# Kernel tuning notes

Measured on AMD Instinct MI355X. Metric: run time of the kernel, lower is better.

The kernel has to match this reference:

```python
import jax, jax.numpy as jnp
import numpy as np

V = 32          # num_variables
T = 48          # num_time_bins
D = 512         # d_model
H = 8           # num_heads
HD = D // H     # head_dim = 64
OD = 16         # observation_dim
B = 4


def setup_inputs() -> dict:
    key = jax.random.key(0)
    ks = jax.random.split(key, 20)
    s = 0.02
    inp = {
        'h': jax.random.normal(ks[0], (B, T, V, D), jnp.float32),
        'observation_state': jax.random.normal(ks[1], (B, T, V, 2), jnp.float32),
        'Wq': jax.random.normal(ks[2], (D, D), jnp.float32) * s,
        'bq': jnp.zeros((D,), jnp.float32),
        'Wk': jax.random.normal(ks[3], (D, D), jnp.float32) * s,
        'bk': jnp.zeros((D,), jnp.float32),
        'Wv': jax.random.normal(ks[4], (D, D), jnp.float32) * s,
        'bv': jnp.zeros((D,), jnp.float32),
        'Wo': jax.random.normal(ks[5], (D, D), jnp.float32) * s,
        'bo': jnp.zeros((D,), jnp.float32),
        'Woq': jax.random.normal(ks[6], (2, H * OD), jnp.float32) * 0.5,
        'boq': jnp.zeros((H * OD,), jnp.float32),
        'Wok': jax.random.normal(ks[7], (2, H * OD), jnp.float32) * 0.5,
        'bok': jnp.zeros((H * OD,), jnp.float32),
        'variable_bias': jax.random.normal(ks[8], (H, V, V), jnp.float32) * 0.01,
        'relative_time_bias': jax.random.normal(ks[9], (H, 2 * T - 1), jnp.float32) * 0.01,
    }
    return inp


def reference(h, observation_state, Wq, bq, Wk, bk, Wv, bv, Wo, bo,
              Woq, boq, Wok, bok, variable_bias, relative_time_bias):
    N = T * V
    scale = 1.0 / np.sqrt(HD)
    obs_scale = 1.0 / np.sqrt(OD)

    # static index buffers (constants)
    flat_var_ids = jnp.tile(jnp.arange(V), T)                       # [N]
    flat_time_ids = jnp.repeat(jnp.arange(T), V)                    # [N]
    rel_index = flat_time_ids[:, None] - flat_time_ids[None, :] + (T - 1)  # [N,N]

    fh = h.reshape(B, N, D)
    fo = observation_state.reshape(B, N, 2)

    def heads(x, nh, hd):
        return x.reshape(B, N, nh, hd).transpose(0, 2, 1, 3)  # [B,H,N,hd]

    q = heads(fh @ Wq + bq, H, HD)
    k = heads(fh @ Wk + bk, H, HD)
    v = heads(fh @ Wv + bv, H, HD)
    oq = heads(fo @ Woq + boq, H, OD)
    ok = heads(fo @ Wok + bok, H, OD)

    content = jnp.einsum('bhnd,bhmd->bhnm', q, k) * scale
    obs = jnp.einsum('bhnd,bhmd->bhnm', oq, ok) * obs_scale
    var_scores = variable_bias[:, flat_var_ids[:, None], flat_var_ids[None, :]]  # [H,N,N]
    time_scores = relative_time_bias[:, rel_index]                                # [H,N,N]

    scores = content + obs + var_scores[None] + time_scores[None]
    attn = jax.nn.softmax(scores, axis=-1)  # dropout off (inference)
    out = jnp.einsum('bhnm,bhmd->bhnd', attn, v)
    out = out.transpose(0, 2, 1, 3).reshape(B, N, D)
    out = out @ Wo + bo
    return out.reshape(B, T, V, D)
```

## Files before the change

### kernel.cpp

```cpp
#include <hip/hip_runtime.h>
#include <math.h>

typedef __bf16 bf16x8 __attribute__((ext_vector_type(8)));
typedef float f32x4 __attribute__((ext_vector_type(4)));

#define NB 4
#define NT 48
#define NV 32
#define ND 512
#define NH 8
#define NN 1536
#define NBN 6144
#define L2E 1.44269504f

#define GLOAD_LDS(g, l) \
    __builtin_amdgcn_global_load_lds( \
        (const __attribute__((address_space(1))) void*)(g), \
        (__attribute__((address_space(3))) void*)(l), 16, 0, 0)

__global__ __launch_bounds__(256) void prep(
    const float* __restrict__ h, const float* __restrict__ obs,
    const float* __restrict__ Wq, const float* __restrict__ Wk,
    const float* __restrict__ Wv, const float* __restrict__ Wo,
    const float* __restrict__ bq, const float* __restrict__ bk,
    const float* __restrict__ bv,
    const float* __restrict__ Wok, const float* __restrict__ bok,
    __bf16* __restrict__ h_bf, __bf16* __restrict__ WcatT,
    __bf16* __restrict__ WoT, float* __restrict__ biascat,
    __bf16* __restrict__ kx)
{
    __shared__ float ts[64][68];
    const int tid = threadIdx.x;
    const int bx = blockIdx.x;
    if (bx < 1536) {
        int t = bx * 256 + tid;
        const float4* src = (const float4*)h + (size_t)t * 2;
        float4 a = src[0], b = src[1];
        __bf16 r[8] = {(__bf16)a.x, (__bf16)a.y, (__bf16)a.z, (__bf16)a.w,
                       (__bf16)b.x, (__bf16)b.y, (__bf16)b.z, (__bf16)b.w};
        *(uint4*)(h_bf + (size_t)t * 8) = *(uint4*)r;
    } else if (bx < 1792) {
        int bw = bx - 1536;
        const int p = bw >> 6, tile = bw & 63;
        const int k0 = (tile >> 3) * 64, c0 = (tile & 7) * 64;
        const float* W = (p == 0) ? Wq : (p == 1) ? Wk : (p == 2) ? Wv : Wo;
        const float scale = (p == 0) ? 0.125f * L2E : 1.0f;
        #pragma unroll
        for (int i = 0; i < 4; i++) {
            int r = (tid >> 4) + i * 16;
            float4 v = *(const float4*)(W + (size_t)(k0 + r) * 512 + c0 + (tid & 15) * 4);
            *(float4*)&ts[r][(tid & 15) * 4] = v;
        }
        __syncthreads();
        __bf16 tmp[16];
        #pragma unroll
        for (int j = 0; j < 16; j++)
            tmp[j] = (__bf16)(ts[(tid & 3) * 16 + j][tid >> 2] * scale);
        int crow = c0 + (tid >> 2);
        __bf16* dst = (p < 3)
            ? WcatT + ((size_t)(p * 512 + crow)) * 512 + k0 + (tid & 3) * 16
            : WoT   + ((size_t)crow) * 512 + k0 + (tid & 3) * 16;
        *(uint4*)dst = *(uint4*)tmp;
        *(uint4*)(dst + 8) = *(uint4*)(tmp + 8);
        if (p < 3 && k0 == 0 && tid < 64) {
            const float* bb = (p == 0) ? bq : (p == 1) ? bk : bv;
            biascat[p * 512 + c0 + tid] = bb[c0 + tid] * scale;
        }
    } else {
        int t = (bx - 1792) * 256 + tid;
        int row = t >> 1, half = t & 1;
        __bf16* dst = kx + (size_t)row * 96 + 64 + half * 16;
        if (half == 0) {
            int bh = row / NN, n = row - bh * NN;
            int b = bh >> 3, hh = bh & 7;
            size_t bn = (size_t)b * NN + n;
            float o0 = obs[bn * 2], o1 = obs[bn * 2 + 1];
            int f = hh * 16;
            __bf16 tmp[16];
            #pragma unroll
            for (int j = 0; j < 16; j++)
                tmp[j] = (__bf16)(o0 * Wok[f + j] + o1 * Wok[128 + f + j] + bok[f + j]);
            *(uint4*)dst       = *(uint4*)tmp;
            *(uint4*)(dst + 8) = *(uint4*)(tmp + 8);
        } else {
            uint4 z = {0, 0, 0, 0};
            *(uint4*)dst       = z;
            *(uint4*)(dst + 8) = z;
        }
    }
}

template<int TM, bool BF16OUT>
__global__ __launch_bounds__(256) void gemm_mfma(
    const __bf16* __restrict__ A, const __bf16* __restrict__ Bt,
    const float* __restrict__ bias, float* __restrict__ Cf,
    __bf16* __restrict__ qarr, __bf16* __restrict__ kx,
    __bf16* __restrict__ vt)
{
    constexpr int MT = TM / 32;
    __shared__ __align__(16) char smem[34816];
    char* const As0 = smem;
    char* const As1 = smem + TM * 64;
    char* const Bs0 = smem + TM * 128;
    char* const Bs1 = smem + TM * 128 + 8192;
    const int tid = threadIdx.x;
    const int w = tid >> 6, lane = tid & 63;
    const int quad = lane >> 4, l16 = lane & 15;
    const int wm = w >> 1, wn = w & 1;
    const int n0 = blockIdx.x * 128, m0 = blockIdx.y * TM;

    const int sm = tid >> 2;
    const int sk = ((tid & 3) ^ ((sm >> 1) & 3)) * 8;
    const __bf16* aptr = A  + (size_t)(m0 + sm) * 512 + sk;
    const __bf16* bptr = Bt + (size_t)(n0 + sm) * 512 + sk;

    f32x4 zero4 = {0.f, 0.f, 0.f, 0.f};
    f32x4 acc[MT][4];
    #pragma unroll
    for (int i = 0; i < MT; i++)
        #pragma unroll
        for (int j = 0; j < 4; j++) acc[i][j] = zero4;

    auto STAGE = [&](char* dA, char* dB, int kt) {
        GLOAD_LDS(aptr + kt, dA + tid * 16);
        if (TM == 128) GLOAD_LDS(aptr + 64 * 512 + kt, dA + 4096 + tid * 16);
        GLOAD_LDS(bptr + kt, dB + tid * 16);
        GLOAD_LDS(bptr + 64 * 512 + kt, dB + 4096 + tid * 16);
    };
    auto COMPUTE = [&](const char* Asb, const char* Bsb) {
        bf16x8 af[MT], bfr[4];
        #pragma unroll
        for (int mt = 0; mt < MT; mt++) {
            int rr = wm * (TM / 2) + mt * 16 + l16;
            af[mt] = *(const bf16x8*)(Asb + rr * 64 + (quad ^ ((rr >> 1) & 3)) * 16);
        }
        #pragma unroll
        for (int nt = 0; nt < 4; nt++) {
            int rr = wn * 64 + nt * 16 + l16;
            bfr[nt] = *(const bf16x8*)(Bsb + rr * 64 + (quad ^ ((rr >> 1) & 3)) * 16);
        }
        #pragma unroll
        for (int mt = 0; mt < MT; mt++)
            #pragma unroll
            for (int nt = 0; nt < 4; nt++)
                acc[mt][nt] = __builtin_amdgcn_mfma_f32_16x16x32_bf16(
                    af[mt], bfr[nt], acc[mt][nt], 0, 0, 0);
    };

    STAGE(As0, Bs0, 0);
    asm volatile("s_waitcnt vmcnt(0)" ::: "memory");
    __builtin_amdgcn_s_barrier();
    for (int kt = 0; kt < 512; kt += 64) {
        STAGE(As1, Bs1, kt + 32);
        COMPUTE(As0, Bs0);
        asm volatile("s_waitcnt vmcnt(0)" ::: "memory");
        __builtin_amdgcn_s_barrier();
        if (kt + 64 < 512) STAGE(As0, Bs0, kt + 64);
        COMPUTE(As1, Bs1);
        asm volatile("s_waitcnt vmcnt(0)" ::: "memory");
        __builtin_amdgcn_s_barrier();
    }

    __syncthreads();
    if (BF16OUT) {
        if (n0 >= 1024) {
            __bf16* CsT = (__bf16*)smem;
            #pragma unroll
            for (int nt = 0; nt < 4; nt++) {
                int cl = wn * 64 + nt * 16 + l16;
                float bia = bias[n0 + cl];
                #pragma unroll
                for (int mt = 0; mt < MT; mt++) {
                    int rl0 = wm * (TM / 2) + mt * 16 + quad * 4;
                    __bf16 pk[4];
                    #pragma unroll
                    for (int r = 0; r < 4; r++)
                        pk[r] = (__bf16)(acc[mt][nt][r] + bia);
                    *(uint2*)&CsT[cl * 136 + rl0] = *(uint2*)pk;
                }
            }
            __syncthreads();
            int cl = tid >> 1, half = tid & 1;
            int f0 = (n0 + cl) & 511;
            int hh = f0 >> 6, d = f0 & 63;
            int dt = d >> 4, l16v = d & 15;
            int bidx = m0 / NN, nm = m0 - bidx * NN;
            int bh = bidx * 8 + hh;
            int mtv = (nm >> 6) + half;
            __bf16* dstb = vt + ((size_t)(bh * 24 + mtv)) * 4096 + l16v * 8;
            #pragma unroll
            for (int j = 0; j < 8; j++) {
                uint4 v = *(uint4*)&CsT[cl * 136 + half * 64 + j * 8];
                int frag = dt * 2 + (j >> 2), qd = j & 3;
                *(uint4*)(dstb + (frag * 4 + qd) * 128) = v;
            }
        } else {
            __bf16* Cs = (__bf16*)smem;
            #pragma unroll
            for (int mt = 0; mt < MT; mt++)
                #pragma unroll
                for (int nt = 0; nt < 4; nt++) {
                    int cl = wn * 64 + nt * 16 + l16;
                    float bia = bias[n0 + cl];
                    #pragma unroll
                    for (int r = 0; r < 4; r++) {
                        int rl = wm * (TM / 2) + mt * 16 + quad * 4 + r;
                        Cs[rl * 132 + cl] = (__bf16)(acc[mt][nt][r] + bia);
                    }
                }
            __syncthreads();
            int rl = tid >> 1, hb = tid & 1;
            int grow = m0 + rl;
            int col0 = n0 + hb * 64;
            int p = col0 >> 9, f0 = col0 & 511, hh = f0 >> 6;
            int bidx = grow / NN, n = grow - bidx * NN;
            __bf16* dst = (p == 0) ? qarr + (size_t)grow * 512 + f0
                                   : kx + ((size_t)(bidx * 8 + hh) * NN + n) * 96;
            #pragma unroll
            for (int j = 0; j < 8; j++) {
                uint2 lo = *(uint2*)&Cs[rl * 132 + hb * 64 + j * 8];
                uint2 hi = *(uint2*)&Cs[rl * 132 + hb * 64 + j * 8 + 4];
                uint4 v = {lo.x, lo.y, hi.x, hi.y};
                *(uint4*)(dst + j * 8) = v;
            }
        }
    } else {
        float* Csf = (float*)smem;
        #pragma unroll
        for (int mt = 0; mt < MT; mt++)
            #pragma unroll
            for (int nt = 0; nt < 4; nt++) {
                int cl = wn * 64 + nt * 16 + l16;
                float bia = bias[n0 + cl];
                #pragma unroll
                for (int r = 0; r < 4; r++) {
                    int rl = wm * (TM / 2) + mt * 16 + quad * 4 + r;
                    Csf[rl * 132 + cl] = acc[mt][nt][r] + bia;
                }
            }
        __syncthreads();
        int rl = tid >> 2, q4 = tid & 3;
        float* dst = Cf + (size_t)(m0 + rl) * 512 + n0 + q4 * 32;
        #pragma unroll
        for (int j = 0; j < 8; j++) {
            uint4 v = *(uint4*)&Csf[rl * 132 + q4 * 32 + j * 4];
            *(uint4*)(dst + j * 4) = v;
        }
    }
}

__global__ __launch_bounds__(256) void attn_mfma(
    const __bf16* __restrict__ qarr, const __bf16* __restrict__ kx,
    const __bf16* __restrict__ vt, const float* __restrict__ obs,
    const float* __restrict__ Woq, const float* __restrict__ boq,
    const float* __restrict__ varb, const float* __restrict__ rtb,
    __bf16* __restrict__ aout)
{
    __shared__ __align__(16) __bf16 Ks[64][128];
    __shared__ __align__(16) __bf16 Ps[64][64];
    __shared__ float rts[96];

    const int tid = threadIdx.x;
    const int w = tid >> 6, lane = tid & 63;
    const int quad = lane >> 4, l16 = lane & 15;
    const int bh = blockIdx.x, qt = blockIdx.y;
    const int b = bh >> 3, h = bh & 7;
    const int n0 = qt * 64;

    if (tid < 95) rts[tid] = rtb[h * 95 + tid] * L2E;

    const int ck = (tid & 15) ^ ((tid >> 4) & 7);
    const __bf16* kbase = kx + (size_t)bh * NN * 96 + ck * 8;
    const __bf16* vtile = vt + (size_t)bh * 24 * 4096 + lane * 8;

    auto STAGE_K = [&](int m0s) {
        #pragma unroll
        for (int i = 0; i < 4; i++) {
            int row = i * 16 + (tid >> 4);
            GLOAD_LDS(kbase + (size_t)(m0s + row) * 96,
                      (char*)Ks + i * 4096 + tid * 16);
        }
    };

    STAGE_K(0);

    const int nl = w * 16 + l16;
    const size_t qrow = (size_t)(b * NN + n0 + nl);
    bf16x8 bq_[3];
    bq_[0] = *(const bf16x8*)(qarr + qrow * 512 + h * 64 + quad * 8);
    bq_[1] = *(const bf16x8*)(qarr + qrow * 512 + h * 64 + 32 + quad * 8);
    {
        uint4 a2u = {0u, 0u, 0u, 0u};
        if (quad < 2) {
            float o0 = obs[qrow * 2], o1 = obs[qrow * 2 + 1];
            int f = h * 16 + quad * 8;
            const float sc = 0.25f * L2E;
            __bf16 tmp[8];
            #pragma unroll
            for (int j = 0; j < 8; j++)
                tmp[j] = (__bf16)(sc * (o0 * Woq[f + j] + o1 * Woq[128 + f + j]
                                        + boq[f + j]));
            a2u = *(uint4*)tmp;
        }
        bq_[2] = *(bf16x8*)&a2u;
    }

    const int rm = (w & 1) * 16 + l16;
    float4 vbA = *(const float4*)(varb + h * 1024 + rm * 32 + quad * 4);
    float4 vbB = *(const float4*)(varb + h * 1024 + rm * 32 + 16 + quad * 4);
    float vA[4] = {vbA.x * L2E, vbA.y * L2E, vbA.z * L2E, vbA.w * L2E};
    float vB[4] = {vbB.x * L2E, vbB.y * L2E, vbB.z * L2E, vbB.w * L2E};
    const int tn = 2 * qt + (w >> 1);

    int wo2[4], ro2[2];
    #pragma unroll
    for (int ct = 0; ct < 4; ct++)
        wo2[ct] = (((ct * 2 + (quad >> 1)) ^ (nl & 7)) * 16) + (quad & 1) * 8;
    #pragma unroll
    for (int ks = 0; ks < 2; ks++)
        ro2[ks] = ((ks * 4 + quad) ^ (nl & 7)) * 16;
    char* psrow = (char*)Ps + nl * 128;

    f32x4 zero4 = {0.f, 0.f, 0.f, 0.f};
    f32x4 o[4];
    f32x4 lpv = zero4;
    #pragma unroll
    for (int i = 0; i < 4; i++) o[i] = zero4;

    asm volatile("s_waitcnt vmcnt(0) lgkmcnt(0)" ::: "memory");
    __builtin_amdgcn_s_barrier();

    for (int mt = 0; mt < 24; mt++) {
        const __bf16* vtm = vtile + (size_t)mt * 4096;
        bf16x8 vfr[4][2];
        #pragma unroll
        for (int dt = 0; dt < 4; dt++)
            #pragma unroll
            for (int ks = 0; ks < 2; ks++)
                vfr[dt][ks] = *(const bf16x8*)(vtm + (dt * 2 + ks) * 512);

        f32x4 sc[4];
        __builtin_amdgcn_s_setprio(1);
        #pragma unroll
        for (int ct = 0; ct < 4; ct++) {
            f32x4 d = zero4;
            int row = ct * 16 + l16;
            #pragma unroll
            for (int ks = 0; ks < 3; ks++) {
                bf16x8 kf = *(const bf16x8*)((const char*)Ks + row * 256
                                + (((ks * 4 + quad) ^ (row & 7)) * 16));
                d = __builtin_amdgcn_mfma_f32_16x16x32_bf16(kf, bq_[ks], d, 0, 0, 0);
            }
            sc[ct] = d;
        }
        __builtin_amdgcn_s_setprio(0);

        asm volatile("s_waitcnt lgkmcnt(0)" ::: "memory");
        __builtin_amdgcn_s_barrier();

        if (mt + 1 < 24) STAGE_K((mt + 1) * 64);

        float tb0 = rts[tn - 2 * mt + 47];
        float tb1 = rts[tn - 2 * mt + 46];
        #pragma unroll
        for (int ct = 0; ct < 4; ct++) {
            float tb = (ct & 2) ? tb1 : tb0;
            const float* vv = (ct & 1) ? vB : vA;
            __bf16 pk[4];
            #pragma unroll
            for (int r = 0; r < 4; r++) {
                float p = exp2f(sc[ct][r] + tb + vv[r]);
                lpv[r] += p;
                pk[r] = (__bf16)p;
            }
            *(uint2*)(psrow + wo2[ct]) = *(uint2*)pk;
        }

        __builtin_amdgcn_s_setprio(1);
        #pragma unroll
        for (int ks = 0; ks < 2; ks++) {
            bf16x8 pf = *(const bf16x8*)(psrow + ro2[ks]);
            #pragma unroll
            for (int dt = 0; dt < 4; dt++)
                o[dt] = __builtin_amdgcn_mfma_f32_16x16x32_bf16(
                    vfr[dt][ks], pf, o[dt], 0, 0, 0);
        }
        __builtin_amdgcn_s_setprio(0);

        asm volatile("s_waitcnt vmcnt(0)" ::: "memory");
        __builtin_amdgcn_s_barrier();
    }

    float lp = (lpv[0] + lpv[1]) + (lpv[2] + lpv[3]);
    lp += __shfl_xor(lp, 16);
    lp += __shfl_xor(lp, 32);
    float inv = 1.0f / lp;
    size_t abase = ((size_t)b * NN + n0 + nl) * 512 + h * 64 + quad * 4;
    #pragma unroll
    for (int dt = 0; dt < 4; dt++) {
        __bf16 ov[4];
        #pragma unroll
        for (int r = 0; r < 4; r++) ov[r] = (__bf16)(o[dt][r] * inv);
        *(uint2*)(aout + abase + dt * 16) = *(uint2*)ov;
    }
}

extern "C" void kernel_launch(void* const* d_in, const int* in_sizes, int n_in,
                              void* d_out, int out_size, void* d_ws, size_t ws_size,
                              hipStream_t stream)
{
    const float* h_   = (const float*)d_in[0];
    const float* obs  = (const float*)d_in[1];
    const float* Wq   = (const float*)d_in[2];
    const float* bq   = (const float*)d_in[3];
    const float* Wk   = (const float*)d_in[4];
    const float* bk   = (const float*)d_in[5];
    const float* Wv   = (const float*)d_in[6];
    const float* bv   = (const float*)d_in[7];
    const float* Wo   = (const float*)d_in[8];
    const float* bo   = (const float*)d_in[9];
    const float* Woq  = (const float*)d_in[10];
    const float* boq  = (const float*)d_in[11];
    const float* Wok  = (const float*)d_in[12];
    const float* bok  = (const float*)d_in[13];
    const float* varb = (const float*)d_in[14];
    const float* rtb  = (const float*)d_in[15];
    float* out = (float*)d_out;

    char* ws = (char*)d_ws;
    __bf16* h_bf    = (__bf16*)ws;                 ws += (size_t)NBN * 512 * 2;
    __bf16* qarr    = (__bf16*)ws;                 ws += (size_t)NBN * 512 * 2;
    __bf16* vt      = (__bf16*)ws;                 ws += (size_t)NBN * 512 * 2;
    __bf16* kx      = (__bf16*)ws;                 ws += ((size_t)32 * NN * 96 + 64) * 2;
    __bf16* attnout = (__bf16*)ws;                 ws += (size_t)NBN * 512 * 2;
    __bf16* WcatT   = (__bf16*)ws;                 ws += (size_t)1536 * 512 * 2;
    __bf16* WoT    = (__bf16*)ws;                  ws += (size_t)512 * 512 * 2;
    float*  biascat = (float*)ws;                  ws += 1536 * 4;

    prep<<<dim3(2176), dim3(256), 0, stream>>>(
        h_, obs, Wq, Wk, Wv, Wo, bq, bk, bv, Wok, bok,
        h_bf, WcatT, WoT, biascat, kx);
    gemm_mfma<128, true><<<dim3(12, 48), dim3(256), 0, stream>>>(
        h_bf, WcatT, biascat, nullptr, qarr, kx, vt);
    attn_mfma<<<dim3(32, 24), dim3(256), 0, stream>>>(qarr, kx, vt, obs, Woq, boq,
                                                      varb, rtb, attnout);
    gemm_mfma<64, false><<<dim3(4, 96), dim3(256), 0, stream>>>(
        attnout, WoT, bo, out, nullptr, nullptr, nullptr);
}
```

Baseline: 181.7 us.

## Split attention keys across waves with register-resident K/V fragments and LDS reduction

Rewrites the attention kernel so each wave handles a different 16-key slice of every key tile across all 64 queries, instead of 16 queries across all keys. K and V are written by the producer kernels in a pre-fragmented layout that each lane loads straight into registers with software prefetch, which removes LDS staging of K and P and the per-iteration barriers. Partial outputs and row sums are reduced across the four waves through LDS at the end. The cost is more registers per thread (four query fragments, sixteen output accumulators) and a serialized final reduction, which may lower occupancy.

```diff
diff --git a/kernel.cpp b/kernel.cpp
--- a/kernel.cpp
+++ b/kernel.cpp
@@ -3,6 +3,7 @@
 
 typedef __bf16 bf16x8 __attribute__((ext_vector_type(8)));
 typedef float f32x4 __attribute__((ext_vector_type(4)));
+typedef short short4v __attribute__((ext_vector_type(4)));
 
 #define NB 4
 #define NT 48
@@ -69,10 +70,13 @@
     } else {
         int t = (bx - 1792) * 256 + tid;
         int row = t >> 1, half = t & 1;
-        __bf16* dst = kx + (size_t)row * 96 + 64 + half * 16;
+        int bh = row / NN, n = row - bh * NN;
+        int mt = n >> 6, wv = (n >> 4) & 3, l16k = n & 15;
+        __bf16* dst = kx + (((size_t)(bh * 24 + mt) * 4 + wv) * 3 + 2) * 512
+                         + (half * 2) * 128 + l16k * 8;
         if (half == 0) {
-            int bh = row / NN, n = row - bh * NN;
-            int b = bh >> 3, hh = bh & 7;
+            int hh = bh & 7;
+            int b = bh >> 3;
             size_t bn = (size_t)b * NN + n;
             float o0 = obs[bn * 2], o1 = obs[bn * 2 + 1];
             int f = hh * 16;
@@ -80,12 +84,12 @@
             #pragma unroll
             for (int j = 0; j < 16; j++)
                 tmp[j] = (__bf16)(o0 * Wok[f + j] + o1 * Wok[128 + f + j] + bok[f + j]);
-            *(uint4*)dst       = *(uint4*)tmp;
-            *(uint4*)(dst + 8) = *(uint4*)(tmp + 8);
+            *(uint4*)dst         = *(uint4*)tmp;
+            *(uint4*)(dst + 128) = *(uint4*)(tmp + 8);
         } else {
             uint4 z = {0, 0, 0, 0};
-            *(uint4*)dst       = z;
-            *(uint4*)(dst + 8) = z;
+            *(uint4*)dst         = z;
+            *(uint4*)(dst + 128) = z;
         }
     }
 }
@@ -187,12 +191,14 @@
             int bidx = m0 / NN, nm = m0 - bidx * NN;
             int bh = bidx * 8 + hh;
             int mtv = (nm >> 6) + half;
-            __bf16* dstb = vt + ((size_t)(bh * 24 + mtv)) * 4096 + l16v * 8;
             #pragma unroll
             for (int j = 0; j < 8; j++) {
                 uint4 v = *(uint4*)&CsT[cl * 136 + half * 64 + j * 8];
-                int frag = dt * 2 + (j >> 2), qd = j & 3;
-                *(uint4*)(dstb + (frag * 4 + qd) * 128) = v;
+                __bf16* pp = (__bf16*)&v;
+                size_t fo = (((size_t)(bh * 24 + mtv) * 4 + (j >> 1)) * 4 + dt) * 256;
+                int q0 = (j & 1) * 2;
+                *(uint2*)(vt + fo + q0 * 64 + l16v * 4)       = *(uint2*)&pp[0];
+                *(uint2*)(vt + fo + (q0 + 1) * 64 + l16v * 4) = *(uint2*)&pp[4];
             }
         } else {
             __bf16* Cs = (__bf16*)smem;
@@ -214,14 +220,25 @@
             int col0 = n0 + hb * 64;
             int p = col0 >> 9, f0 = col0 & 511, hh = f0 >> 6;
             int bidx = grow / NN, n = grow - bidx * NN;
-            __bf16* dst = (p == 0) ? qarr + (size_t)grow * 512 + f0
-                                   : kx + ((size_t)(bidx * 8 + hh) * NN + n) * 96;
-            #pragma unroll
-            for (int j = 0; j < 8; j++) {
-                uint2 lo = *(uint2*)&Cs[rl * 132 + hb * 64 + j * 8];
-                uint2 hi = *(uint2*)&Cs[rl * 132 + hb * 64 + j * 8 + 4];
-                uint4 v = {lo.x, lo.y, hi.x, hi.y};
-                *(uint4*)(dst + j * 8) = v;
+            if (p == 0) {
+                __bf16* dst = qarr + (size_t)grow * 512 + f0;
+                #pragma unroll
+                for (int j = 0; j < 8; j++) {
+                    uint2 lo = *(uint2*)&Cs[rl * 132 + hb * 64 + j * 8];
+                    uint2 hi = *(uint2*)&Cs[rl * 132 + hb * 64 + j * 8 + 4];
+                    uint4 v = {lo.x, lo.y, hi.x, hi.y};
+                    *(uint4*)(dst + j * 8) = v;
+                }
+            } else {
+                int mtk = n >> 6, wv = (n >> 4) & 3, l16k = n & 15;
+                size_t fb = ((size_t)((bidx * 8 + hh) * 24 + mtk) * 4 + wv) * 1536;
+                #pragma unroll
+                for (int j = 0; j < 8; j++) {
+                    uint2 lo = *(uint2*)&Cs[rl * 132 + hb * 64 + j * 8];
+                    uint2 hi = *(uint2*)&Cs[rl * 132 + hb * 64 + j * 8 + 4];
+                    uint4 v = {lo.x, lo.y, hi.x, hi.y};
+                    *(uint4*)(kx + fb + (j >> 2) * 512 + (j & 3) * 128 + l16k * 8) = v;
+                }
             }
         }
     } else {
@@ -256,9 +273,9 @@
     const float* __restrict__ varb, const float* __restrict__ rtb,
     __bf16* __restrict__ aout)
 {
-    __shared__ __align__(16) __bf16 Ks[64][128];
-    __shared__ __align__(16) __bf16 Ps[64][64];
-    __shared__ float rts[96];
+    __shared__ float Or[64][68];
+    __shared__ float lps[4][64];
+    __shared__ float2 rts2[96];
 
     const int tid = threadIdx.x;
     const int w = tid >> 6, lane = tid & 63;
@@ -267,142 +284,158 @@
     const int b = bh >> 3, h = bh & 7;
     const int n0 = qt * 64;
 
-    if (tid < 95) rts[tid] = rtb[h * 95 + tid] * L2E;
-
-    const int ck = (tid & 15) ^ ((tid >> 4) & 7);
-    const __bf16* kbase = kx + (size_t)bh * NN * 96 + ck * 8;
-    const __bf16* vtile = vt + (size_t)bh * 24 * 4096 + lane * 8;
-
-    auto STAGE_K = [&](int m0s) {
-        #pragma unroll
-        for (int i = 0; i < 4; i++) {
-            int row = i * 16 + (tid >> 4);
-            GLOAD_LDS(kbase + (size_t)(m0s + row) * 96,
-                      (char*)Ks + i * 4096 + tid * 16);
-        }
-    };
-
-    STAGE_K(0);
-
-    const int nl = w * 16 + l16;
-    const size_t qrow = (size_t)(b * NN + n0 + nl);
-    bf16x8 bq_[3];
-    bq_[0] = *(const bf16x8*)(qarr + qrow * 512 + h * 64 + quad * 8);
-    bq_[1] = *(const bf16x8*)(qarr + qrow * 512 + h * 64 + 32 + quad * 8);
-    {
+    if (tid < 95) {
+        float a = rtb[h * 95 + tid] * L2E;
+        float c = (tid < 94) ? rtb[h * 95 + tid + 1] * L2E : 0.f;
+        rts2[tid].x = a;
+        rts2[tid].y = c;
+    }
+
+    const __bf16* kwb = kx + ((size_t)bh * 24 * 4 + w) * 1536 + lane * 8;
+    const __bf16* vwb = vt + ((size_t)bh * 24 * 4 + w) * 1024 + lane * 4;
+
+    bf16x8 qf[4][3];
+    #pragma unroll
+    for (int nt = 0; nt < 4; nt++) {
+        const size_t qrow = (size_t)(b * NN + n0 + nt * 16 + l16);
+        qf[nt][0] = *(const bf16x8*)(qarr + qrow * 512 + h * 64 + quad * 8);
+        qf[nt][1] = *(const bf16x8*)(qarr + qrow * 512 + h * 64 + 32 + quad * 8);
         uint4 a2u = {0u, 0u, 0u, 0u};
         if (quad < 2) {
             float o0 = obs[qrow * 2], o1 = obs[qrow * 2 + 1];
             int f = h * 16 + quad * 8;
-            const float sc = 0.25f * L2E;
+            const float scq = 0.25f * L2E;
             __bf16 tmp[8];
             #pragma unroll
             for (int j = 0; j < 8; j++)
-                tmp[j] = (__bf16)(sc * (o0 * Woq[f + j] + o1 * Woq[128 + f + j]
-                                        + boq[f + j]));
+                tmp[j] = (__bf16)(scq * (o0 * Woq[f + j] + o1 * Woq[128 + f + j]
+                                         + boq[f + j]));
             a2u = *(uint4*)tmp;
         }
-        bq_[2] = *(bf16x8*)&a2u;
-    }
-
-    const int rm = (w & 1) * 16 + l16;
-    float4 vbA = *(const float4*)(varb + h * 1024 + rm * 32 + quad * 4);
-    float4 vbB = *(const float4*)(varb + h * 1024 + rm * 32 + 16 + quad * 4);
-    float vA[4] = {vbA.x * L2E, vbA.y * L2E, vbA.z * L2E, vbA.w * L2E};
-    float vB[4] = {vbB.x * L2E, vbB.y * L2E, vbB.z * L2E, vbB.w * L2E};
-    const int tn = 2 * qt + (w >> 1);
-
-    int wo2[4], ro2[2];
-    #pragma unroll
-    for (int ct = 0; ct < 4; ct++)
-        wo2[ct] = (((ct * 2 + (quad >> 1)) ^ (nl & 7)) * 16) + (quad & 1) * 8;
-    #pragma unroll
-    for (int ks = 0; ks < 2; ks++)
-        ro2[ks] = ((ks * 4 + quad) ^ (nl & 7)) * 16;
-    char* psrow = (char*)Ps + nl * 128;
+        qf[nt][2] = *(bf16x8*)&a2u;
+    }
+
+    const float* vbp = varb + h * 1024 + (w & 1) * 16 + quad * 4;
+    f32x4 vvA = *(const f32x4*)(vbp + l16 * 32);
+    f32x4 vvB = *(const f32x4*)(vbp + (16 + l16) * 32);
+    vvA *= L2E; vvB *= L2E;
+
+    const int rbase = 2 * qt - (w >> 1) + 47;
 
     f32x4 zero4 = {0.f, 0.f, 0.f, 0.f};
-    f32x4 o[4];
-    f32x4 lpv = zero4;
-    #pragma unroll
-    for (int i = 0; i < 4; i++) o[i] = zero4;
-
-    asm volatile("s_waitcnt vmcnt(0) lgkmcnt(0)" ::: "memory");
-    __builtin_amdgcn_s_barrier();
+    f32x4 o_p[4][4];
+    #pragma unroll
+    for (int i = 0; i < 4; i++)
+        #pragma unroll
+        for (int j = 0; j < 4; j++) o_p[i][j] = zero4;
+    float lp_s[4] = {0.f, 0.f, 0.f, 0.f};
+
+    bf16x8 kc[3]; short4v vc[4];
+    #pragma unroll
+    for (int ks = 0; ks < 3; ks++) kc[ks] = *(const bf16x8*)(kwb + ks * 512);
+    #pragma unroll
+    for (int dt = 0; dt < 4; dt++) vc[dt] = *(const short4v*)(vwb + dt * 256);
+
+    __syncthreads();
 
     for (int mt = 0; mt < 24; mt++) {
-        const __bf16* vtm = vtile + (size_t)mt * 4096;
-        bf16x8 vfr[4][2];
-        #pragma unroll
-        for (int dt = 0; dt < 4; dt++)
-            #pragma unroll
-            for (int ks = 0; ks < 2; ks++)
-                vfr[dt][ks] = *(const bf16x8*)(vtm + (dt * 2 + ks) * 512);
+        bf16x8 kn[3]; short4v vn[4];
+        if (mt + 1 < 24) {
+            const __bf16* kp = kwb + (size_t)(mt + 1) * 6144;
+            const __bf16* vp = vwb + (size_t)(mt + 1) * 4096;
+            #pragma unroll
+            for (int ks = 0; ks < 3; ks++) kn[ks] = *(const bf16x8*)(kp + ks * 512);
+            #pragma unroll
+            for (int dt = 0; dt < 4; dt++) vn[dt] = *(const short4v*)(vp + dt * 256);
+        }
 
         f32x4 sc[4];
         __builtin_amdgcn_s_setprio(1);
         #pragma unroll
-        for (int ct = 0; ct < 4; ct++) {
+        for (int nt = 0; nt < 4; nt++) {
             f32x4 d = zero4;
-            int row = ct * 16 + l16;
-            #pragma unroll
-            for (int ks = 0; ks < 3; ks++) {
-                bf16x8 kf = *(const bf16x8*)((const char*)Ks + row * 256
-                                + (((ks * 4 + quad) ^ (row & 7)) * 16));
-                d = __builtin_amdgcn_mfma_f32_16x16x32_bf16(kf, bq_[ks], d, 0, 0, 0);
+            #pragma unroll
+            for (int ks = 0; ks < 3; ks++)
+                d = __builtin_amdgcn_mfma_f32_16x16x32_bf16(kc[ks], qf[nt][ks], d, 0, 0, 0);
+            sc[nt] = d;
+        }
+        __builtin_amdgcn_s_setprio(0);
+
+        float2 tb = rts2[rbase - 2 * mt];
+        short4v pf[4];
+        #pragma unroll
+        for (int nt = 0; nt < 4; nt++) {
+            float tbx = (nt < 2) ? tb.x : tb.y;
+            const f32x4& vv = (nt & 1) ? vvB : vvA;
+            union { __bf16 e[4]; short4v s; } pk;
+            #pragma unroll
+            for (int r = 0; r < 4; r++) {
+                float p = exp2f(sc[nt][r] + vv[r] + tbx);
+                lp_s[nt] += p;
+                pk.e[r] = (__bf16)p;
             }
-            sc[ct] = d;
-        }
+            pf[nt] = pk.s;
+        }
+
+        __builtin_amdgcn_s_setprio(1);
+        #pragma unroll
+        for (int nt = 0; nt < 4; nt++)
+            #pragma unroll
+            for (int dt = 0; dt < 4; dt++)
+                o_p[dt][nt] = __builtin_amdgcn_mfma_f32_16x16x16bf16_1k(
+                    vc[dt], pf[nt], o_p[dt][nt], 0, 0, 0);
         __builtin_amdgcn_s_setprio(0);
 
-        asm volatile("s_waitcnt lgkmcnt(0)" ::: "memory");
-        __builtin_amdgcn_s_barrier();
-
-        if (mt + 1 < 24) STAGE_K((mt + 1) * 64);
-
-        float tb0 = rts[tn - 2 * mt + 47];
-        float tb1 = rts[tn - 2 * mt + 46];
-        #pragma unroll
-        for (int ct = 0; ct < 4; ct++) {
-            float tb = (ct & 2) ? tb1 : tb0;
-            const float* vv = (ct & 1) ? vB : vA;
-            __bf16 pk[4];
-            #pragma unroll
-            for (int r = 0; r < 4; r++) {
-                float p = exp2f(sc[ct][r] + tb + vv[r]);
-                lpv[r] += p;
-                pk[r] = (__bf16)p;
-            }
-            *(uint2*)(psrow + wo2[ct]) = *(uint2*)pk;
-        }
-
-        __builtin_amdgcn_s_setprio(1);
-        #pragma unroll
-        for (int ks = 0; ks < 2; ks++) {
-            bf16x8 pf = *(const bf16x8*)(psrow + ro2[ks]);
+        if (mt + 1 < 24) {
+            #pragma unroll
+            for (int ks = 0; ks < 3; ks++) kc[ks] = kn[ks];
+            #pragma unroll
+            for (int dt = 0; dt < 4; dt++) vc[dt] = vn[dt];
+        }
+    }
+
+    #pragma unroll
+    for (int nt = 0; nt < 4; nt++) {
+        lp_s[nt] += __shfl_xor(lp_s[nt], 16);
+        lp_s[nt] += __shfl_xor(lp_s[nt], 32);
+    }
+    if (quad == 0) {
+        #pragma unroll
+        for (int nt = 0; nt < 4; nt++) lps[w][nt * 16 + l16] = lp_s[nt];
+    }
+
+    #pragma unroll
+    for (int ws = 0; ws < 4; ws++) {
+        if (w == ws) {
             #pragma unroll
             for (int dt = 0; dt < 4; dt++)
-                o[dt] = __builtin_amdgcn_mfma_f32_16x16x32_bf16(
-                    vfr[dt][ks], pf, o[dt], 0, 0, 0);
-        }
-        __builtin_amdgcn_s_setprio(0);
-
-        asm volatile("s_waitcnt vmcnt(0)" ::: "memory");
-        __builtin_amdgcn_s_barrier();
-    }
-
-    float lp = (lpv[0] + lpv[1]) + (lpv[2] + lpv[3]);
-    lp += __shfl_xor(lp, 16);
-    lp += __shfl_xor(lp, 32);
-    float inv = 1.0f / lp;
-    size_t abase = ((size_t)b * NN + n0 + nl) * 512 + h * 64 + quad * 4;
-    #pragma unroll
-    for (int dt = 0; dt < 4; dt++) {
-        __bf16 ov[4];
-        #pragma unroll
-        for (int r = 0; r < 4; r++) ov[r] = (__bf16)(o[dt][r] * inv);
-        *(uint2*)(aout + abase + dt * 16) = *(uint2*)ov;
-    }
+                #pragma unroll
+                for (int nt = 0; nt < 4; nt++) {
+                    float* dst = &Or[nt * 16 + l16][dt * 16 + quad * 4];
+                    if (ws == 0) *(f32x4*)dst = o_p[dt][nt];
+                    else {
+                        f32x4 t = *(f32x4*)dst;
+                        *(f32x4*)dst = t + o_p[dt][nt];
+                    }
+                }
+        }
+        __syncthreads();
+    }
+
+    int n = tid >> 2, dq = tid & 3;
+    float linv = 1.0f / (lps[0][n] + lps[1][n] + lps[2][n] + lps[3][n]);
+    __bf16 ov[16];
+    #pragma unroll
+    for (int jj = 0; jj < 4; jj++) {
+        f32x4 t = *(f32x4*)&Or[n][dq * 16 + jj * 4];
+        ov[jj * 4 + 0] = (__bf16)(t[0] * linv);
+        ov[jj * 4 + 1] = (__bf16)(t[1] * linv);
+        ov[jj * 4 + 2] = (__bf16)(t[2] * linv);
+        ov[jj * 4 + 3] = (__bf16)(t[3] * linv);
+    }
+    size_t abase = ((size_t)(b * NN) + n0 + n) * 512 + h * 64 + dq * 16;
+    *(uint4*)(aout + abase)     = *(uint4*)&ov[0];
+    *(uint4*)(aout + abase + 8) = *(uint4*)&ov[8];
 }
 
 extern "C" void kernel_launch(void* const* d_in, const int* in_sizes, int n_in,
@@ -434,7 +467,7 @@
     __bf16* kx      = (__bf16*)ws;                 ws += ((size_t)32 * NN * 96 + 64) * 2;
     __bf16* attnout = (__bf16*)ws;                 ws += (size_t)NBN * 512 * 2;
     __bf16* WcatT   = (__bf16*)ws;                 ws += (size_t)1536 * 512 * 2;
-    __bf16* WoT    = (__bf16*)ws;                  ws += (size_t)512 * 512 * 2;
+    __bf16* WoT     = (__bf16*)ws;                 ws += (size_t)512 * 512 * 2;
     float*  biascat = (float*)ws;                  ws += 1536 * 4;
 
     prep<<<dim3(2176), dim3(256), 0, stream>>>(
```

Result: slower. 186.3 us (+2.5%).

## Keep P in registers via 16x16x16 MFMA, double-buffer K tiles, MFMA row-sum

Applied to the files above, without the earlier changes.

The attention kernel stops writing softmax probabilities to LDS and reading them back. It instead feeds the QK accumulator registers directly as the B operand of 16x16x16 bf16 MFMAs, and the V-transpose layout written by the QKV GEMM is changed to match. K tiles are now double-buffered in LDS, processing two 64-key tiles per barrier pair. The softmax denominator is computed with an MFMA against a ones vector instead of shuffles. The trade-offs are twice as many smaller MFMA instructions, more LDS for K, and a launch-bounds occupancy hint.

```diff
diff --git a/kernel.cpp b/kernel.cpp
--- a/kernel.cpp
+++ b/kernel.cpp
@@ -3,6 +3,8 @@
 
 typedef __bf16 bf16x8 __attribute__((ext_vector_type(8)));
 typedef float f32x4 __attribute__((ext_vector_type(4)));
+typedef short short4v __attribute__((ext_vector_type(4)));
+typedef short short8v __attribute__((ext_vector_type(8)));
 
 #define NB 4
 #define NT 48
@@ -187,12 +189,15 @@
             int bidx = m0 / NN, nm = m0 - bidx * NN;
             int bh = bidx * 8 + hh;
             int mtv = (nm >> 6) + half;
-            __bf16* dstb = vt + ((size_t)(bh * 24 + mtv)) * 4096 + l16v * 8;
             #pragma unroll
             for (int j = 0; j < 8; j++) {
                 uint4 v = *(uint4*)&CsT[cl * 136 + half * 64 + j * 8];
-                int frag = dt * 2 + (j >> 2), qd = j & 3;
-                *(uint4*)(dstb + (frag * 4 + qd) * 128) = v;
+                __bf16* pp = (__bf16*)&v;
+                int q0 = (j & 1) * 2;
+                size_t fo = ((size_t)(bh * 24 + mtv) * 8 + (j >> 1) * 2 + (dt >> 1)) * 512
+                            + (dt & 1) * 4 + l16v * 8;
+                *(uint2*)(vt + fo + q0 * 128)       = *(uint2*)&pp[0];
+                *(uint2*)(vt + fo + (q0 + 1) * 128) = *(uint2*)&pp[4];
             }
         } else {
             __bf16* Cs = (__bf16*)smem;
@@ -249,15 +254,14 @@
     }
 }
 
-__global__ __launch_bounds__(256) void attn_mfma(
+__global__ __launch_bounds__(256, 3) void attn_mfma(
     const __bf16* __restrict__ qarr, const __bf16* __restrict__ kx,
     const __bf16* __restrict__ vt, const float* __restrict__ obs,
     const float* __restrict__ Woq, const float* __restrict__ boq,
     const float* __restrict__ varb, const float* __restrict__ rtb,
     __bf16* __restrict__ aout)
 {
-    __shared__ __align__(16) __bf16 Ks[64][128];
-    __shared__ __align__(16) __bf16 Ps[64][64];
+    __shared__ __align__(16) __bf16 Ks[2][64][128];
     __shared__ float rts[96];
 
     const int tid = threadIdx.x;
@@ -271,18 +275,18 @@
 
     const int ck = (tid & 15) ^ ((tid >> 4) & 7);
     const __bf16* kbase = kx + (size_t)bh * NN * 96 + ck * 8;
-    const __bf16* vtile = vt + (size_t)bh * 24 * 4096 + lane * 8;
-
-    auto STAGE_K = [&](int m0s) {
+    auto STAGE_K = [&](int p, int m0s) {
         #pragma unroll
         for (int i = 0; i < 4; i++) {
             int row = i * 16 + (tid >> 4);
             GLOAD_LDS(kbase + (size_t)(m0s + row) * 96,
-                      (char*)Ks + i * 4096 + tid * 16);
-        }
-    };
-
-    STAGE_K(0);
+                      (char*)Ks + p * 16384 + i * 4096 + tid * 16);
+        }
+    };
+    STAGE_K(0, 0);
+    STAGE_K(1, 64);
+
+    const __bf16* vwb = vt + (size_t)bh * 24 * 4096 + lane * 8;
 
     const int nl = w * 16 + l16;
     const size_t qrow = (size_t)(b * NN + n0 + nl);
@@ -312,34 +316,18 @@
     float vB[4] = {vbB.x * L2E, vbB.y * L2E, vbB.z * L2E, vbB.w * L2E};
     const int tn = 2 * qt + (w >> 1);
 
-    int wo2[4], ro2[2];
+    union { __bf16 e[4]; short4v s; } one_u;
     #pragma unroll
-    for (int ct = 0; ct < 4; ct++)
-        wo2[ct] = (((ct * 2 + (quad >> 1)) ^ (nl & 7)) * 16) + (quad & 1) * 8;
+    for (int j = 0; j < 4; j++) one_u.e[j] = (__bf16)1.0f;
+    const short4v ones = one_u.s;
+
+    f32x4 zero4 = {0.f, 0.f, 0.f, 0.f};
+    f32x4 o_p[4];
+    f32x4 lpa = zero4;
     #pragma unroll
-    for (int ks = 0; ks < 2; ks++)
-        ro2[ks] = ((ks * 4 + quad) ^ (nl & 7)) * 16;
-    char* psrow = (char*)Ps + nl * 128;
-
-    f32x4 zero4 = {0.f, 0.f, 0.f, 0.f};
-    f32x4 o[4];
-    f32x4 lpv = zero4;
-    #pragma unroll
-    for (int i = 0; i < 4; i++) o[i] = zero4;
-
-    asm volatile("s_waitcnt vmcnt(0) lgkmcnt(0)" ::: "memory");
-    __builtin_amdgcn_s_barrier();
-
-    for (int mt = 0; mt < 24; mt++) {
-        const __bf16* vtm = vtile + (size_t)mt * 4096;
-        bf16x8 vfr[4][2];
-        #pragma unroll
-        for (int dt = 0; dt < 4; dt++)
-            #pragma unroll
-            for (int ks = 0; ks < 2; ks++)
-                vfr[dt][ks] = *(const bf16x8*)(vtm + (dt * 2 + ks) * 512);
-
-        f32x4 sc[4];
+    for (int i = 0; i < 4; i++) o_p[i] = zero4;
+
+    auto QK = [&](int p, f32x4* sc) {
         __builtin_amdgcn_s_setprio(1);
         #pragma unroll
         for (int ct = 0; ct < 4; ct++) {
@@ -347,60 +335,88 @@
             int row = ct * 16 + l16;
             #pragma unroll
             for (int ks = 0; ks < 3; ks++) {
-                bf16x8 kf = *(const bf16x8*)((const char*)Ks + row * 256
-                                + (((ks * 4 + quad) ^ (row & 7)) * 16));
+                bf16x8 kf = *(const bf16x8*)((const char*)Ks + p * 16384
+                                + row * 256 + (((ks * 4 + quad) ^ (row & 7)) * 16));
                 d = __builtin_amdgcn_mfma_f32_16x16x32_bf16(kf, bq_[ks], d, 0, 0, 0);
             }
             sc[ct] = d;
         }
         __builtin_amdgcn_s_setprio(0);
-
-        asm volatile("s_waitcnt lgkmcnt(0)" ::: "memory");
-        __builtin_amdgcn_s_barrier();
-
-        if (mt + 1 < 24) STAGE_K((mt + 1) * 64);
-
+    };
+    auto SM = [&](const f32x4* sc, int mt, short4v* pf) {
         float tb0 = rts[tn - 2 * mt + 47];
         float tb1 = rts[tn - 2 * mt + 46];
         #pragma unroll
         for (int ct = 0; ct < 4; ct++) {
             float tb = (ct & 2) ? tb1 : tb0;
             const float* vv = (ct & 1) ? vB : vA;
-            __bf16 pk[4];
-            #pragma unroll
-            for (int r = 0; r < 4; r++) {
-                float p = exp2f(sc[ct][r] + tb + vv[r]);
-                lpv[r] += p;
-                pk[r] = (__bf16)p;
-            }
-            *(uint2*)(psrow + wo2[ct]) = *(uint2*)pk;
-        }
-
+            union { __bf16 e[4]; short4v s; } pk;
+            #pragma unroll
+            for (int r = 0; r < 4; r++)
+                pk.e[r] = (__bf16)exp2f(sc[ct][r] + tb + vv[r]);
+            pf[ct] = pk.s;
+        }
+    };
+    auto PV = [&](const short8v* vfr, const short4v* pf) {
         __builtin_amdgcn_s_setprio(1);
         #pragma unroll
-        for (int ks = 0; ks < 2; ks++) {
-            bf16x8 pf = *(const bf16x8*)(psrow + ro2[ks]);
-            #pragma unroll
-            for (int dt = 0; dt < 4; dt++)
-                o[dt] = __builtin_amdgcn_mfma_f32_16x16x32_bf16(
-                    vfr[dt][ks], pf, o[dt], 0, 0, 0);
+        for (int ct = 0; ct < 4; ct++) {
+            lpa = __builtin_amdgcn_mfma_f32_16x16x16bf16_1k(ones, pf[ct], lpa, 0, 0, 0);
+            #pragma unroll
+            for (int dt = 0; dt < 4; dt++) {
+                short8v v8 = vfr[ct * 2 + (dt >> 1)];
+                short4v va = (dt & 1)
+                    ? __builtin_shufflevector(v8, v8, 4, 5, 6, 7)
+                    : __builtin_shufflevector(v8, v8, 0, 1, 2, 3);
+                o_p[dt] = __builtin_amdgcn_mfma_f32_16x16x16bf16_1k(
+                    va, pf[ct], o_p[dt], 0, 0, 0);
+            }
         }
         __builtin_amdgcn_s_setprio(0);
-
-        asm volatile("s_waitcnt vmcnt(0)" ::: "memory");
-        __builtin_amdgcn_s_barrier();
-    }
-
-    float lp = (lpv[0] + lpv[1]) + (lpv[2] + lpv[3]);
-    lp += __shfl_xor(lp, 16);
-    lp += __shfl_xor(lp, 32);
-    float inv = 1.0f / lp;
-    size_t abase = ((size_t)b * NN + n0 + nl) * 512 + h * 64 + quad * 4;
+    };
+
+    __syncthreads();
+
+    for (int i = 0; i < 12; i++) {
+        const int mt0 = 2 * i;
+        short8v v0[8];
+        {
+            const __bf16* vp = vwb + (size_t)mt0 * 4096;
+            #pragma unroll
+            for (int fi = 0; fi < 8; fi++)
+                v0[fi] = *(const short8v*)(vp + fi * 512);
+        }
+        f32x4 sc0[4], sc1[4];
+        QK(0, sc0);
+        QK(1, sc1);
+        __syncthreads();
+        if (i < 11) {
+            STAGE_K(0, (mt0 + 2) * 64);
+            STAGE_K(1, (mt0 + 3) * 64);
+        }
+        short4v p0[4];
+        SM(sc0, mt0, p0);
+        short8v v1[8];
+        {
+            const __bf16* vp = vwb + (size_t)(mt0 + 1) * 4096;
+            #pragma unroll
+            for (int fi = 0; fi < 8; fi++)
+                v1[fi] = *(const short8v*)(vp + fi * 512);
+        }
+        PV(v0, p0);
+        short4v p1[4];
+        SM(sc1, mt0 + 1, p1);
+        PV(v1, p1);
+        __syncthreads();
+    }
+
+    float linv = 1.0f / lpa[0];
+    size_t abase = ((size_t)(b * NN) + n0 + nl) * 512 + h * 64 + quad * 4;
     #pragma unroll
     for (int dt = 0; dt < 4; dt++) {
         __bf16 ov[4];
         #pragma unroll
-        for (int r = 0; r < 4; r++) ov[r] = (__bf16)(o[dt][r] * inv);
+        for (int r = 0; r < 4; r++) ov[r] = (__bf16)(o_p[dt][r] * linv);
         *(uint2*)(aout + abase + dt * 16) = *(uint2*)ov;
     }
 }
@@ -434,7 +450,7 @@
     __bf16* kx      = (__bf16*)ws;                 ws += ((size_t)32 * NN * 96 + 64) * 2;
     __bf16* attnout = (__bf16*)ws;                 ws += (size_t)NBN * 512 * 2;
     __bf16* WcatT   = (__bf16*)ws;                 ws += (size_t)1536 * 512 * 2;
-    __bf16* WoT    = (__bf16*)ws;                  ws += (size_t)512 * 512 * 2;
+    __bf16* WoT     = (__bf16*)ws;                 ws += (size_t)512 * 512 * 2;
     float*  biascat = (float*)ws;                  ws += 1536 * 4;
 
     prep<<<dim3(2176), dim3(256), 0, stream>>>(
```

Result: faster. 177.7 us (median of 2 runs) (-2.2%).
